# Optimization experiments

Measured on AMD Instinct MI355X. Metric: run time of the kernel, lower is better.

The kernel has to match this reference:

```python
import jax, jax.numpy as jnp
import numpy as np

N = 100000          # num nodes
E = 3200000         # num edges (avg degree 32)
C = 64              # num_classes
L = 10000           # num labeled nodes
NUM_LAYERS = 10
ALPHA = 0.9


def setup_inputs() -> dict:
    key = jax.random.key(0)
    k1, k2, k3, k4 = jax.random.split(key, 4)
    y_soft = jax.random.normal(k1, (N, C), dtype=jnp.float32)
    y_true = jax.random.randint(k2, (L,), 0, C)
    mask = jax.random.randint(k3, (L,), 0, N)
    edge_index = jax.random.randint(k4, (2, E), 0, N)
    return {"y_soft": y_soft, "y_true": y_true, "mask": mask,
            "edge_index": edge_index}


def reference(y_soft, y_true, mask, edge_index):
    row, col = edge_index[0], edge_index[1]  # source -> target

    # smooth(): normalize predictions, then clamp labeled nodes to one-hot y
    z = jax.nn.softmax(y_soft, axis=1)                       # [N, C]
    y_onehot = jax.nn.one_hot(y_true, C, dtype=z.dtype)      # [L, C]
    z = z.at[mask].set(y_onehot)

    # gcn_norm without self-loops: w_e = deg^-1/2[row] * deg^-1/2[col]
    ones = jnp.ones((edge_index.shape[1],), dtype=z.dtype)
    deg = jax.ops.segment_sum(ones, col, num_segments=N)     # [N]
    dinv = jnp.where(deg > 0,
                     jax.lax.rsqrt(jnp.maximum(deg, 1e-12)),
                     jnp.zeros_like(deg))
    norm = dinv[row] * dinv[col]                             # [E]

    # Label spreading: Z <- clip(alpha * (D^-1/2 A D^-1/2) Z + (1-alpha) Z0, 0, 1)
    res = (1.0 - ALPHA) * z
    out = z
    for _ in range(NUM_LAYERS):
        msg = norm[:, None] * out[row]                       # [E, C] gather
        agg = jax.ops.segment_sum(msg, col, num_segments=N)  # [N, C] scatter-add
        out = jnp.clip(ALPHA * agg + res, 0.0, 1.0)          # PyG post_step clamp
    return out
```

## Files before the change

### kernel.cpp

```cpp
#include <hip/hip_runtime.h>
#include <hip/hip_fp16.h>

#define NCLS 64
#define ALPHA 0.9f
#define SCAN_BS 256
#define SCAN_CHUNK 1024
#define NBUCK 256
#define BSHIFT 9
#define BSPAN 512
#define P1_CAP 3200
#define ROWMASK 0x7FFFFFu

__device__ __forceinline__ float wave_max64(float v) {
    #pragma unroll
    for (int o = 32; o > 0; o >>= 1) v = fmaxf(v, __shfl_xor(v, o, 64));
    return v;
}
__device__ __forceinline__ float wave_sum64(float v) {
    #pragma unroll
    for (int o = 32; o > 0; o >>= 1) v += __shfl_xor(v, o, 64);
    return v;
}

__global__ void winner_k(const int* __restrict__ mask, int* __restrict__ winner, int L) {
    int i = blockIdx.x * blockDim.x + threadIdx.x;
    if (i < L) atomicMax(&winner[mask[i]], i);
}

__global__ void bcount_k(const int* __restrict__ col, int* __restrict__ bcnt, int E) {
    __shared__ int h[NBUCK];
    int t = threadIdx.x;
    h[t] = 0;
    __syncthreads();
    int stride = gridDim.x * blockDim.x;
    for (int e = blockIdx.x * blockDim.x + t; e < E; e += stride)
        atomicAdd(&h[col[e] >> BSHIFT], 1);
    __syncthreads();
    if (h[t]) atomicAdd(&bcnt[t], h[t]);
}

__global__ void bscan_k(const int* __restrict__ bcnt, int* __restrict__ bbase,
                        int* __restrict__ bcur, int E) {
    __shared__ int lds[NBUCK];
    int t = threadIdx.x;
    int v = bcnt[t];
    lds[t] = v;
    __syncthreads();
    for (int o = 1; o < NBUCK; o <<= 1) {
        int x = (t >= o) ? lds[t - o] : 0;
        __syncthreads();
        lds[t] += x;
        __syncthreads();
    }
    int ex = lds[t] - v;
    bbase[t] = ex;
    bcur[t] = ex;
    if (t == NBUCK - 1) bbase[NBUCK] = E;
}

__global__ void binpass1_k(const int* __restrict__ row, const int* __restrict__ col,
                           int* __restrict__ bcur, unsigned* __restrict__ bpk,
                           int E, int chunk) {
    __shared__ int hist[NBUCK];
    __shared__ int scn[NBUCK];
    __shared__ int lbase[NBUCK];
    __shared__ int lcur[NBUCK];
    __shared__ unsigned pay[P1_CAP];
    __shared__ unsigned char bkt[P1_CAP];
    int t = threadIdx.x;
    int e0 = blockIdx.x * chunk;
    int e1 = min(e0 + chunk, E);
    if (e0 >= E) return;
    hist[t] = 0;
    __syncthreads();
    for (int e = e0 + t; e < e1; e += 256)
        atomicAdd(&hist[col[e] >> BSHIFT], 1);
    __syncthreads();
    scn[t] = hist[t];
    __syncthreads();
    for (int o = 1; o < 256; o <<= 1) {
        int y = (t >= o) ? scn[t - o] : 0;
        __syncthreads();
        scn[t] += y;
        __syncthreads();
    }
    int cnt = hist[t];
    int lstart = scn[t] - cnt;
    int gb = 0;
    if (cnt > 0) gb = atomicAdd(&bcur[t], cnt);
    lbase[t] = gb - lstart;
    lcur[t] = lstart;
    __syncthreads();
    for (int e = e0 + t; e < e1; e += 256) {
        int c = col[e];
        int b = c >> BSHIFT;
        int p = atomicAdd(&lcur[b], 1);
        pay[p] = ((unsigned)(c & (BSPAN - 1)) << 23) | (unsigned)row[e];
        bkt[p] = (unsigned char)b;
    }
    __syncthreads();
    int n = e1 - e0;
    for (int i = t; i < n; i += 256) {
        unsigned w = pay[i];
        int b = bkt[i];
        bpk[lbase[b] + i] = w;
    }
}

__global__ void bdeg_k(const int* __restrict__ bbase, const unsigned* __restrict__ bpk,
                       int* __restrict__ deg, float* __restrict__ dinv, int Nn) {
    __shared__ int hist[BSPAN];
    int b = blockIdx.x;
    int nb0 = b * BSPAN;
    if (nb0 >= Nn) return;
    int t = threadIdx.x;
    hist[t] = 0;
    hist[t + 256] = 0;
    __syncthreads();
    int e0 = bbase[b];
    int e1 = bbase[b + 1];
    for (int e = e0 + t; e < e1; e += 256)
        atomicAdd(&hist[bpk[e] >> 23], 1);
    __syncthreads();
    int n0 = nb0 + t;
    if (n0 < Nn) {
        int d = hist[t];
        deg[n0] = d;
        dinv[n0] = (d > 0) ? rsqrtf((float)d) : 0.0f;
    }
    int n1 = nb0 + 256 + t;
    if (n1 < Nn) {
        int d = hist[t + 256];
        deg[n1] = d;
        dinv[n1] = (d > 0) ? rsqrtf((float)d) : 0.0f;
    }
}

__global__ void scan_local_k(const int* __restrict__ deg, int* __restrict__ rowptr,
                             int* __restrict__ bsum, int n) {
    __shared__ int lds[SCAN_BS];
    int base = blockIdx.x * SCAN_CHUNK;
    int t = threadIdx.x;
    int v[4];
    int s = 0;
    #pragma unroll
    for (int k = 0; k < 4; ++k) {
        int i = base + t * 4 + k;
        v[k] = (i < n) ? deg[i] : 0;
        s += v[k];
    }
    lds[t] = s;
    __syncthreads();
    for (int o = 1; o < SCAN_BS; o <<= 1) {
        int x = (t >= o) ? lds[t - o] : 0;
        __syncthreads();
        lds[t] += x;
        __syncthreads();
    }
    int ex = (t > 0) ? lds[t - 1] : 0;
    #pragma unroll
    for (int k = 0; k < 4; ++k) {
        int i = base + t * 4 + k;
        if (i < n) rowptr[i] = ex;
        ex += v[k];
    }
    if (t == SCAN_BS - 1) bsum[blockIdx.x] = lds[t];
}

__global__ void scan_bsum_k(int* __restrict__ bsum, int nb) {
    __shared__ int lds[SCAN_BS];
    int t = threadIdx.x;
    int v = (t < nb) ? bsum[t] : 0;
    lds[t] = v;
    __syncthreads();
    for (int o = 1; o < SCAN_BS; o <<= 1) {
        int x = (t >= o) ? lds[t - o] : 0;
        __syncthreads();
        lds[t] += x;
        __syncthreads();
    }
    if (t < nb) bsum[t] = lds[t] - v;
}

__global__ void scan_add_k(int* __restrict__ rowptr, const int* __restrict__ bsum, int n) {
    int i = blockIdx.x * blockDim.x + threadIdx.x;
    if (i < n) rowptr[i] += bsum[i / SCAN_CHUNK];
}

__global__ void binpass2_k(const int* __restrict__ rowptr, const unsigned* __restrict__ bpk,
                           int* __restrict__ src, int Nn, int E) {
    __shared__ int cur[BSPAN];
    int b = blockIdx.x;
    int nb0 = b * BSPAN;
    if (nb0 >= Nn) return;
    int nb1 = min(nb0 + BSPAN, Nn);
    int t = threadIdx.x;
    for (int i = nb0 + t; i < nb1; i += 256) cur[i - nb0] = rowptr[i];
    __syncthreads();
    int e0 = rowptr[nb0];
    int e1 = (nb1 < Nn) ? rowptr[nb1] : E;
    for (int e = e0 + t; e < e1; e += 256) {
        unsigned w = bpk[e];
        int p = atomicAdd(&cur[w >> 23], 1);
        src[p] = (int)(w & ROWMASK);
    }
}

__global__ void init_k(const float* __restrict__ y, const int* __restrict__ winner,
                       const int* __restrict__ ytrue, const float* __restrict__ dinv,
                       __half* __restrict__ res_h, __half* __restrict__ vh, int Nn) {
    int lane = threadIdx.x & 63;
    int wave = (blockIdx.x * blockDim.x + threadIdx.x) >> 6;
    int nwaves = (gridDim.x * blockDim.x) >> 6;
    for (int n = wave; n < Nn; n += nwaves) {
        float v = y[(size_t)n * NCLS + lane];
        float m = wave_max64(v);
        float e = expf(v - m);
        float s = wave_sum64(e);
        float u = e / s;
        int w = winner[n];
        if (w >= 0) u = (lane == ytrue[w]) ? 1.0f : 0.0f;
        res_h[(size_t)n * NCLS + lane] = __float2half((1.0f - ALPHA) * u);
        vh[(size_t)n * NCLS + lane] = __float2half(dinv[n] * u);
    }
}

__global__ void pull_k(const int* __restrict__ rowptr, const int* __restrict__ deg,
                       const int* __restrict__ src, const float* __restrict__ dinv,
                       const __half2* __restrict__ vin2, const __half2* __restrict__ res2,
                       __half2* __restrict__ vout2, float2* __restrict__ uout2,
                       int n_nodes, int last) {
    int lane = threadIdx.x & 63;
    int half_id = lane >> 5;
    int k = lane & 31;
    int n = (blockIdx.x * blockDim.x + threadIdx.x) >> 6;
    if (n >= n_nodes) return;
    int start = rowptr[n];
    int len = deg[n];
    float2 a0 = make_float2(0.f, 0.f), a1 = make_float2(0.f, 0.f);
    float2 a2 = make_float2(0.f, 0.f), a3 = make_float2(0.f, 0.f);
    for (int base = 0; base < len; base += 64) {
        int m = min(64, len - base);
        int sv = (lane < m) ? __builtin_nontemporal_load(&src[start + base + lane]) : 0;
        int j = 0;
        for (; j + 8 <= m; j += 8) {
            int sA = __shfl(sv, j     + half_id, 64);
            int sB = __shfl(sv, j + 2 + half_id, 64);
            int sC = __shfl(sv, j + 4 + half_id, 64);
            int sD = __shfl(sv, j + 6 + half_id, 64);
            float2 fA = __half22float2(vin2[(size_t)sA * 32 + k]);
            float2 fB = __half22float2(vin2[(size_t)sB * 32 + k]);
            float2 fC = __half22float2(vin2[(size_t)sC * 32 + k]);
            float2 fD = __half22float2(vin2[(size_t)sD * 32 + k]);
            a0.x += fA.x; a0.y += fA.y;
            a1.x += fB.x; a1.y += fB.y;
            a2.x += fC.x; a2.y += fC.y;
            a3.x += fD.x; a3.y += fD.y;
        }
        for (; j + 2 <= m; j += 2) {
            int sA = __shfl(sv, j + half_id, 64);
            float2 fA = __half22float2(vin2[(size_t)sA * 32 + k]);
            a0.x += fA.x; a0.y += fA.y;
        }
        if (j < m) {
            int sA = __shfl(sv, j, 64);
            float2 fA = __half22float2(vin2[(size_t)sA * 32 + k]);
            if (half_id == 0) { a0.x += fA.x; a0.y += fA.y; }
        }
    }
    float sx = (a0.x + a1.x) + (a2.x + a3.x);
    float sy = (a0.y + a1.y) + (a2.y + a3.y);
    sx += __shfl_xor(sx, 32, 64);
    sy += __shfl_xor(sy, 32, 64);
    float di = dinv[n];
    unsigned rraw = __builtin_nontemporal_load(
        reinterpret_cast<const unsigned*>(&res2[(size_t)n * 32 + k]));
    union { unsigned u; __half2 h; } cv; cv.u = rraw;
    float2 r = __half22float2(cv.h);
    float u0 = fminf(fmaxf(ALPHA * (di * sx) + r.x, 0.0f), 1.0f);
    float u1 = fminf(fmaxf(ALPHA * (di * sy) + r.y, 0.0f), 1.0f);
    if (lane < 32) {
        size_t idx = (size_t)n * 32 + k;
        if (last) uout2[idx] = make_float2(u0, u1);
        else      vout2[idx] = __floats2half2_rn(di * u0, di * u1);
    }
}

extern "C" void kernel_launch(void* const* d_in, const int* in_sizes, int n_in,
                              void* d_out, int out_size, void* d_ws, size_t ws_size,
                              hipStream_t stream) {
    const float* y_soft = (const float*)d_in[0];
    const int* y_true  = (const int*)d_in[1];
    const int* mask    = (const int*)d_in[2];
    const int* edge    = (const int*)d_in[3];

    const int NC = in_sizes[0];
    const int Nn = NC / NCLS;
    const int L  = in_sizes[1];
    const int E  = in_sizes[3] / 2;

    const int* row = edge;
    const int* col = edge + E;

    float2* uout2 = (float2*)d_out;

    char* ws = (char*)d_ws;
    size_t off = 0;
    auto alloc = [&](size_t bytes) { char* p = ws + off; off += (bytes + 255) & ~(size_t)255; return p; };
    size_t reg0 = (size_t)E * 4;
    size_t vh_bytes = (size_t)NC * 2;
    if (2 * vh_bytes > reg0) reg0 = 2 * vh_bytes;
    char* region0 = alloc(reg0);
    unsigned* bpk = (unsigned*)region0;
    __half* vhA   = (__half*)region0;
    __half* vhB   = (__half*)(region0 + vh_bytes);
    __half* res_h = (__half*)alloc((size_t)NC * 2);
    int*   src    = (int*)alloc((size_t)E * 4);
    int*   deg    = (int*)alloc((size_t)Nn * 4);
    int*   rowptr = (int*)alloc((size_t)Nn * 4);
    float* dinv   = (float*)alloc((size_t)Nn * 4);
    int*   winner = (int*)alloc((size_t)Nn * 4);
    int*   bcnt   = (int*)alloc((size_t)NBUCK * 4);
    int*   bbase  = (int*)alloc((size_t)(NBUCK + 1) * 4);
    int*   bcur   = (int*)alloc((size_t)NBUCK * 4);
    int*   bsum   = (int*)alloc((size_t)SCAN_BS * 4);

    const int NB = (Nn + SCAN_CHUNK - 1) / SCAN_CHUNK;
    const int NBK = (Nn + BSPAN - 1) / BSPAN;

    hipMemsetAsync(winner, 0xFF, (size_t)Nn * 4, stream);
    hipMemsetAsync(bcnt, 0, (size_t)NBUCK * 4, stream);

    winner_k<<<(L + 255) / 256, 256, 0, stream>>>(mask, winner, L);

    bcount_k<<<1024, 256, 0, stream>>>(col, bcnt, E);
    bscan_k<<<1, NBUCK, 0, stream>>>(bcnt, bbase, bcur, E);
    const int chunk = P1_CAP;
    const int nchunks = (E + chunk - 1) / chunk;
    binpass1_k<<<nchunks, 256, 0, stream>>>(row, col, bcur, bpk, E, chunk);
    bdeg_k<<<NBK, 256, 0, stream>>>(bbase, bpk, deg, dinv, Nn);
    scan_local_k<<<NB, SCAN_BS, 0, stream>>>(deg, rowptr, bsum, Nn);
    scan_bsum_k<<<1, SCAN_BS, 0, stream>>>(bsum, NB);
    scan_add_k<<<(Nn + 255) / 256, 256, 0, stream>>>(rowptr, bsum, Nn);
    binpass2_k<<<NBK, 256, 0, stream>>>(rowptr, bpk, src, Nn, E);

    init_k<<<2048, 256, 0, stream>>>(y_soft, winner, y_true, dinv, res_h, vhA, Nn);

    const int pull_blocks = (Nn * NCLS + 255) / 256;
    for (int it = 0; it < 10; ++it) {
        const __half2* vin2 = (const __half2*)((it & 1) ? vhB : vhA);
        __half2* vout2      = (__half2*)((it & 1) ? vhA : vhB);
        pull_k<<<pull_blocks, 256, 0, stream>>>(rowptr, deg, src, dinv,
                                                vin2, (const __half2*)res_h,
                                                vout2, uout2, Nn, it == 9);
    }
}
```

Before: 863.7 us.

## Process nodes in degree-sorted order and widen gather unroll in pull kernel

```diff
diff --git a/kernel.cpp b/kernel.cpp
--- a/kernel.cpp
+++ b/kernel.cpp
@@ -203,6 +203,33 @@
         unsigned w = bpk[e];
         int p = atomicAdd(&cur[w >> 23], 1);
         src[p] = (int)(w & ROWMASK);
+    }
+}
+
+__global__ void dhist_k(const int* __restrict__ deg, int* __restrict__ dh, int Nn) {
+    int i = blockIdx.x * blockDim.x + threadIdx.x;
+    if (i < Nn) atomicAdd(&dh[255 - min(deg[i], 255)], 1);
+}
+__global__ void dscan_k(int* __restrict__ dh, int* __restrict__ dcur) {
+    __shared__ int lds[256];
+    int t = threadIdx.x;
+    int v = dh[t];
+    lds[t] = v;
+    __syncthreads();
+    for (int o = 1; o < 256; o <<= 1) {
+        int x = (t >= o) ? lds[t - o] : 0;
+        __syncthreads();
+        lds[t] += x;
+        __syncthreads();
+    }
+    dcur[t] = lds[t] - v;
+}
+__global__ void dperm_k(const int* __restrict__ deg, int* __restrict__ dcur,
+                        int* __restrict__ perm, int Nn) {
+    int i = blockIdx.x * blockDim.x + threadIdx.x;
+    if (i < Nn) {
+        int p = atomicAdd(&dcur[255 - min(deg[i], 255)], 1);
+        perm[p] = i;
     }
 }
 
@@ -225,51 +252,56 @@
     }
 }
 
+#define GATHER(dst, s) do {                                                      \
+    float2 f_ = __half22float2(vin2[(size_t)(s) * 32 + k]);                      \
+    dst.x += f_.x; dst.y += f_.y;                                                \
+} while (0)
+
 __global__ void pull_k(const int* __restrict__ rowptr, const int* __restrict__ deg,
                        const int* __restrict__ src, const float* __restrict__ dinv,
+                       const int* __restrict__ perm,
                        const __half2* __restrict__ vin2, const __half2* __restrict__ res2,
                        __half2* __restrict__ vout2, float2* __restrict__ uout2,
                        int n_nodes, int last) {
     int lane = threadIdx.x & 63;
     int half_id = lane >> 5;
     int k = lane & 31;
-    int n = (blockIdx.x * blockDim.x + threadIdx.x) >> 6;
-    if (n >= n_nodes) return;
+    int wv = (blockIdx.x * blockDim.x + threadIdx.x) >> 6;
+    if (wv >= n_nodes) return;
+    int n = perm[wv];
     int start = rowptr[n];
     int len = deg[n];
     float2 a0 = make_float2(0.f, 0.f), a1 = make_float2(0.f, 0.f);
     float2 a2 = make_float2(0.f, 0.f), a3 = make_float2(0.f, 0.f);
+    float2 a4 = make_float2(0.f, 0.f), a5 = make_float2(0.f, 0.f);
+    float2 a6 = make_float2(0.f, 0.f), a7 = make_float2(0.f, 0.f);
     for (int base = 0; base < len; base += 64) {
         int m = min(64, len - base);
         int sv = (lane < m) ? __builtin_nontemporal_load(&src[start + base + lane]) : 0;
         int j = 0;
-        for (; j + 8 <= m; j += 8) {
-            int sA = __shfl(sv, j     + half_id, 64);
-            int sB = __shfl(sv, j + 2 + half_id, 64);
-            int sC = __shfl(sv, j + 4 + half_id, 64);
-            int sD = __shfl(sv, j + 6 + half_id, 64);
-            float2 fA = __half22float2(vin2[(size_t)sA * 32 + k]);
-            float2 fB = __half22float2(vin2[(size_t)sB * 32 + k]);
-            float2 fC = __half22float2(vin2[(size_t)sC * 32 + k]);
-            float2 fD = __half22float2(vin2[(size_t)sD * 32 + k]);
-            a0.x += fA.x; a0.y += fA.y;
-            a1.x += fB.x; a1.y += fB.y;
-            a2.x += fC.x; a2.y += fC.y;
-            a3.x += fD.x; a3.y += fD.y;
+        for (; j + 16 <= m; j += 16) {
+            int s0 = __shfl(sv, j      + half_id, 64);
+            int s1 = __shfl(sv, j + 2  + half_id, 64);
+            int s2 = __shfl(sv, j + 4  + half_id, 64);
+            int s3 = __shfl(sv, j + 6  + half_id, 64);
+            int s4 = __shfl(sv, j + 8  + half_id, 64);
+            int s5 = __shfl(sv, j + 10 + half_id, 64);
+            int s6 = __shfl(sv, j + 12 + half_id, 64);
+            int s7 = __shfl(sv, j + 14 + half_id, 64);
+            GATHER(a0, s0); GATHER(a1, s1); GATHER(a2, s2); GATHER(a3, s3);
+            GATHER(a4, s4); GATHER(a5, s5); GATHER(a6, s6); GATHER(a7, s7);
         }
         for (; j + 2 <= m; j += 2) {
-            int sA = __shfl(sv, j + half_id, 64);
-            float2 fA = __half22float2(vin2[(size_t)sA * 32 + k]);
-            a0.x += fA.x; a0.y += fA.y;
+            int s0 = __shfl(sv, j + half_id, 64);
+            GATHER(a0, s0);
         }
         if (j < m) {
-            int sA = __shfl(sv, j, 64);
-            float2 fA = __half22float2(vin2[(size_t)sA * 32 + k]);
-            if (half_id == 0) { a0.x += fA.x; a0.y += fA.y; }
+            int s0 = __shfl(sv, j, 64);
+            if (half_id == 0) GATHER(a0, s0);
         }
     }
-    float sx = (a0.x + a1.x) + (a2.x + a3.x);
-    float sy = (a0.y + a1.y) + (a2.y + a3.y);
+    float sx = ((a0.x + a1.x) + (a2.x + a3.x)) + ((a4.x + a5.x) + (a6.x + a7.x));
+    float sy = ((a0.y + a1.y) + (a2.y + a3.y)) + ((a4.y + a5.y) + (a6.y + a7.y));
     sx += __shfl_xor(sx, 32, 64);
     sy += __shfl_xor(sy, 32, 64);
     float di = dinv[n];
@@ -281,8 +313,14 @@
     float u1 = fminf(fmaxf(ALPHA * (di * sy) + r.y, 0.0f), 1.0f);
     if (lane < 32) {
         size_t idx = (size_t)n * 32 + k;
-        if (last) uout2[idx] = make_float2(u0, u1);
-        else      vout2[idx] = __floats2half2_rn(di * u0, di * u1);
+        if (last) {
+            union { float2 f; unsigned long long b; } cf; cf.f = make_float2(u0, u1);
+            __builtin_nontemporal_store(cf.b, reinterpret_cast<unsigned long long*>(&uout2[idx]));
+        } else {
+            __half2 hv = __floats2half2_rn(di * u0, di * u1);
+            union { __half2 h; unsigned b; } ch; ch.h = hv;
+            __builtin_nontemporal_store(ch.b, reinterpret_cast<unsigned*>(&vout2[idx]));
+        }
     }
 }
 
@@ -320,16 +358,20 @@
     int*   rowptr = (int*)alloc((size_t)Nn * 4);
     float* dinv   = (float*)alloc((size_t)Nn * 4);
     int*   winner = (int*)alloc((size_t)Nn * 4);
+    int*   perm   = (int*)alloc((size_t)Nn * 4);
     int*   bcnt   = (int*)alloc((size_t)NBUCK * 4);
     int*   bbase  = (int*)alloc((size_t)(NBUCK + 1) * 4);
     int*   bcur   = (int*)alloc((size_t)NBUCK * 4);
     int*   bsum   = (int*)alloc((size_t)SCAN_BS * 4);
+    int*   dh     = (int*)alloc(256 * 4);
+    int*   dcur   = (int*)alloc(256 * 4);
 
     const int NB = (Nn + SCAN_CHUNK - 1) / SCAN_CHUNK;
     const int NBK = (Nn + BSPAN - 1) / BSPAN;
 
     hipMemsetAsync(winner, 0xFF, (size_t)Nn * 4, stream);
     hipMemsetAsync(bcnt, 0, (size_t)NBUCK * 4, stream);
+    hipMemsetAsync(dh, 0, 256 * 4, stream);
 
     winner_k<<<(L + 255) / 256, 256, 0, stream>>>(mask, winner, L);
 
@@ -344,13 +386,17 @@
     scan_add_k<<<(Nn + 255) / 256, 256, 0, stream>>>(rowptr, bsum, Nn);
     binpass2_k<<<NBK, 256, 0, stream>>>(rowptr, bpk, src, Nn, E);
 
+    dhist_k<<<(Nn + 255) / 256, 256, 0, stream>>>(deg, dh, Nn);
+    dscan_k<<<1, 256, 0, stream>>>(dh, dcur);
+    dperm_k<<<(Nn + 255) / 256, 256, 0, stream>>>(deg, dcur, perm, Nn);
+
     init_k<<<2048, 256, 0, stream>>>(y_soft, winner, y_true, dinv, res_h, vhA, Nn);
 
     const int pull_blocks = (Nn * NCLS + 255) / 256;
     for (int it = 0; it < 10; ++it) {
         const __half2* vin2 = (const __half2*)((it & 1) ? vhB : vhA);
         __half2* vout2      = (__half2*)((it & 1) ? vhA : vhB);
-        pull_k<<<pull_blocks, 256, 0, stream>>>(rowptr, deg, src, dinv,
+        pull_k<<<pull_blocks, 256, 0, stream>>>(rowptr, deg, src, dinv, perm,
                                                 vin2, (const __half2*)res_h,
                                                 vout2, uout2, Nn, it == 9);
     }
```

New measurement: 1.281 ms. +48.3%, slower.
